# Performance work log

Measured on AMD Instinct MI355X. Metric: run time of the kernel, lower is better.

## Reference

```python
import jax, jax.numpy as jnp
import numpy as np

V = 100000          # vocab size
D = 256             # hidden dim
B, N = 32, 128      # batch, max_len
K = 100             # noise_ratio
NORM_TERM = 11.512925  # log(V), norm_term='auto'
BACKOFF_PROB = 1e-10


def setup_inputs() -> dict:
    key = jax.random.key(0)
    ks = jax.random.split(key, 6)
    target = jax.random.randint(ks[0], (B, N), 0, V)
    noise_samples = jax.random.randint(ks[1], (B, N, K), 0, V)
    hidden = jax.random.normal(ks[2], (B, N, D), dtype=jnp.float32) * 0.1
    weight = jax.random.normal(ks[3], (V, D), dtype=jnp.float32) * 0.05
    bias = jax.random.normal(ks[4], (V,), dtype=jnp.float32) * 0.01
    u = jax.random.uniform(ks[5], (V,), dtype=jnp.float32) + BACKOFF_PROB
    noise_probs = u / jnp.sum(u)  # normalized noise distribution
    return {"target": target, "noise_samples": noise_samples, "hidden": hidden,
            "weight": weight, "bias": bias, "noise_probs": noise_probs}


def reference(target, noise_samples, hidden, weight, bias, noise_probs):
    # score_noise = log P_noise(noise_samples)   (B,N,K) -- irregular gather on (V,)
    score_noise = jnp.log(noise_probs)[noise_samples]
    # get_score (IndexLinear): gathered output-embedding dot products
    w_t = weight[target]                                   # (B,N,D)
    score_model = jnp.einsum('bnd,bnd->bn', hidden, w_t) + bias[target] - NORM_TERM
    w_n = weight[noise_samples]                            # (B,N,K,D) big gather
    score_noise_in_model = (jnp.einsum('bnd,bnkd->bnk', hidden, w_n)
                            + bias[noise_samples] - NORM_TERM)
    # NCE binary classification loss (score_target_in_noise passed as zeros)
    log_k = jnp.log(jnp.float32(K))
    logit_true = score_model - log_k                        # (B,N) label=1
    logit_noise = score_noise_in_model - score_noise - log_k  # (B,N,K) label=0
    # BCE-with-logits: -log sigmoid(x) = softplus(-x); -log(1-sigmoid(x)) = softplus(x)
    loss = jax.nn.softplus(-logit_true) + jnp.sum(jax.nn.softplus(logit_noise), axis=-1)
    # reduction='elementwise_mean'
    return jnp.mean(loss)
```

## Files before the change

kernel.cpp:

```cpp
#include <hip/hip_runtime.h>
#include <math.h>

#define V 100000
#define D 256
#define B 32
#define N 128
#define K 100
#define NPOS (B * N)
#define NPAIR (NPOS * (K + 1))
#define BIN_ROWS 32
#define NBIN (V / BIN_ROWS)
#define NSHARD 16
#define CAP_S 32
#define MAXTOT (NSHARD * CAP_S)
#define ROW_W32 136
#define HVEC (NPOS * D / 4)
#define NORM_TERM 11.512925f
#define LOG_K 4.605170186f

typedef float    f32x4 __attribute__((ext_vector_type(4)));
typedef unsigned u32x2 __attribute__((ext_vector_type(2)));
typedef unsigned u32x4 __attribute__((ext_vector_type(4)));
typedef __fp16   f16x2 __attribute__((ext_vector_type(2)));

__device__ __forceinline__ float softplus(float x) {
    return fmaxf(x, 0.f) + __logf(1.f + __expf(-fabsf(x)));
}

__device__ __forceinline__ unsigned pack_f16(float a, float b) {
#if __has_builtin(__builtin_amdgcn_cvt_pkrtz)
    f16x2 h = __builtin_amdgcn_cvt_pkrtz(a, b);
#else
    f16x2 h; h.x = (__fp16)a; h.y = (__fp16)b;
#endif
    union { f16x2 h; unsigned u; } c; c.h = h;
    return c.u;
}

#if __has_builtin(__builtin_amdgcn_fdot2)
#define DOT2(a, b, c) __builtin_amdgcn_fdot2((a), (b), (c), false)
#else
__device__ __forceinline__ float DOT2(f16x2 a, f16x2 b, float c) {
    return fmaf((float)a.x, (float)b.x, fmaf((float)a.y, (float)b.y, c));
}
#endif

union V4H { u32x4 u; f16x2 h[4]; };

template <int CTRL>
__device__ __forceinline__ float dpp_add(float x) {
    int y = __builtin_amdgcn_update_dpp(__float_as_int(x), __float_as_int(x),
                                        CTRL, 0xF, 0xF, false);
    return x + __int_as_float(y);
}
__device__ __forceinline__ float quarter_sum(float x) {
    x = dpp_add<0xB1>(x);
    x = dpp_add<0x4E>(x);
    x = dpp_add<0x141>(x);
    x = dpp_add<0x140>(x);
    return x;
}

__global__ __launch_bounds__(256) void scatter_hconv_kernel(
    const int* __restrict__ target, const int* __restrict__ noise,
    const float* __restrict__ hidden,
    int* __restrict__ cursor, unsigned* __restrict__ buf,
    unsigned* __restrict__ htab32)
{
    const int p = blockIdx.x * 256 + threadIdx.x;

    int row, pos; unsigned flag;
    if (p < NPOS * K) { pos = p / K; row = noise[p]; flag = 0u; }
    else              { pos = p - NPOS * K; row = target[pos]; flag = 1u; }
    const int cell = (row >> 5) * NSHARD + (blockIdx.x & (NSHARD - 1));
    const int slot = atomicAdd(&cursor[cell], 1);
    if (slot < CAP_S)
        buf[(size_t)cell * CAP_S + slot] =
            ((unsigned)(row & (BIN_ROWS - 1)) << 13) | ((unsigned)pos << 1) | flag;

    if (p < HVEC) {
        const f32x4 h4 = *((const f32x4*)hidden + p);
        u32x2 o;
        o.x = pack_f16(h4.x, h4.y);
        o.y = pack_f16(h4.z, h4.w);
        *(u32x2*)(htab32 + (size_t)p * 2) = o;
    }
}

__global__ __launch_bounds__(256, 8) void compute_kernel(
    const unsigned* __restrict__ htab32, const float* __restrict__ weight,
    const float* __restrict__ bias, const float* __restrict__ noise_probs,
    const int* __restrict__ cursor, const unsigned* __restrict__ buf,
    float* __restrict__ out)
{
    __shared__ unsigned slab32[BIN_ROWS * ROW_W32];
    __shared__ float    sbias[BIN_ROWS];
    __shared__ float    slogp[BIN_ROWS];
    __shared__ unsigned plist[MAXTOT];
    __shared__ int      scnt[NSHARD];
    __shared__ int      pref[NSHARD + 1];
    __shared__ float    wsum[4];

    const int bin = blockIdx.x;
    const int tid = threadIdx.x;

    if (tid < NSHARD)
        scnt[tid] = min(cursor[bin * NSHARD + tid], CAP_S);
    __syncthreads();
    if (tid == 0) {
        int s = 0;
        #pragma unroll
        for (int i = 0; i < NSHARD; ++i) { pref[i] = s; s += scnt[i]; }
        pref[NSHARD] = s;
    }
    __syncthreads();
    const int total = pref[NSHARD];
    if (total == 0) return;

    const int wave = tid >> 6;
    const int lane = tid & 63;
    const int q    = lane >> 4;
    const int ql   = lane & 15;
    const int row0 = bin * BIN_ROWS;

    for (int r = wave; r < BIN_ROWS; r += 4) {
        const f32x4 w4 = __builtin_nontemporal_load(
            (const f32x4*)(weight + (size_t)(row0 + r) * D + lane * 4));
        u32x2 o;
        o.x = pack_f16(w4.x, w4.y);
        o.y = pack_f16(w4.z, w4.w);
        *(u32x2*)(slab32 + r * ROW_W32 + lane * 2) = o;
    }
    if (tid < BIN_ROWS) {
        sbias[tid] = bias[row0 + tid];
        slogp[tid] = __logf(noise_probs[row0 + tid]);
    }
    for (int i = tid; i < total; i += 256) {
        int s = 0;
        #pragma unroll
        for (int j = 1; j < NSHARD; ++j) s += (i >= pref[j]);
        plist[i] = buf[((size_t)(bin * NSHARD + s)) * CAP_S + (i - pref[s])];
    }
    __syncthreads();

    float loss = 0.f;
    for (int base = wave * 4; base < total; base += 16) {
        const int p = base + q;
        const bool valid = (p < total);
        const unsigned rec = valid ? plist[p] : 0u;
        const int rloc = (int)((rec >> 13) & (BIN_ROWS - 1));
        const int pos  = (int)((rec >> 1) & (NPOS - 1));

        const u32x4* hp = (const u32x4*)(htab32 + (size_t)pos * 128) + ql;
        V4H H0, H1, W0, W1;
        H0.u = hp[0];
        H1.u = hp[16];
        const unsigned* wr = slab32 + rloc * ROW_W32;
        W0.u = *(const u32x4*)(wr + ql * 4);
        W1.u = *(const u32x4*)(wr + 64 + ql * 4);

        float a0 = 0.f, a1 = 0.f, a2 = 0.f, a3 = 0.f;
        a0 = DOT2(H0.h[0], W0.h[0], a0);
        a1 = DOT2(H0.h[1], W0.h[1], a1);
        a2 = DOT2(H0.h[2], W0.h[2], a2);
        a3 = DOT2(H0.h[3], W0.h[3], a3);
        a0 = DOT2(H1.h[0], W1.h[0], a0);
        a1 = DOT2(H1.h[1], W1.h[1], a1);
        a2 = DOT2(H1.h[2], W1.h[2], a2);
        a3 = DOT2(H1.h[3], W1.h[3], a3);

        const float r = quarter_sum((a0 + a1) + (a2 + a3));

        const float score = r + sbias[rloc] - NORM_TERM;
        const float x = (rec & 1u) ? (LOG_K - score)
                                   : (score - slogp[rloc] - LOG_K);
        if (valid && ql == 0) loss += softplus(x);
    }

    loss += __shfl_xor(loss, 16, 64);
    loss += __shfl_xor(loss, 32, 64);
    if (lane == 0) wsum[wave] = loss;
    __syncthreads();
    if (tid == 0)
        atomicAdd(out, (wsum[0] + wsum[1] + wsum[2] + wsum[3])
                       * (1.0f / (float)NPOS));
}

extern "C" void kernel_launch(void* const* d_in, const int* in_sizes, int n_in,
                              void* d_out, int out_size, void* d_ws, size_t ws_size,
                              hipStream_t stream) {
    const int*   target      = (const int*)d_in[0];
    const int*   noise       = (const int*)d_in[1];
    const float* hidden      = (const float*)d_in[2];
    const float* weight      = (const float*)d_in[3];
    const float* bias        = (const float*)d_in[4];
    const float* noise_probs = (const float*)d_in[5];
    float* out = (float*)d_out;

    const size_t cursor_bytes = (size_t)NBIN * NSHARD * 4;
    const size_t buf_bytes    = (size_t)NBIN * NSHARD * CAP_S * 4;
    int*      cursor = (int*)d_ws;
    unsigned* buf    = (unsigned*)((char*)d_ws + cursor_bytes);
    unsigned* htab32 = (unsigned*)((char*)d_ws + cursor_bytes + buf_bytes);

    (void)hipMemsetAsync(cursor, 0, cursor_bytes, stream);
    (void)hipMemsetAsync(out, 0, sizeof(float), stream);

    scatter_hconv_kernel<<<NPAIR / 256, 256, 0, stream>>>(
        target, noise, hidden, cursor, buf, htab32);
    compute_kernel<<<NBIN, 256, 0, stream>>>(
        htab32, weight, bias, noise_probs, cursor, buf, out);
}
```

Before: 220.7 us.

## Process three bins per block with register-prefetched next weight slab

Each compute block now handles three consecutive bins instead of one. While it computes the current bin, it prefetches the next bin's weight rows and pair records into registers, then writes them to shared memory after a barrier. This is meant to hide global-load latency and cut per-block setup and launch overhead. In exchange it adds register pressure (occupancy bound lowered from 8 to 6 blocks), two barriers per bin and fewer blocks in the grid, and blocks can no longer exit early when a bin is empty.

```diff
diff --git a/kernel.cpp b/kernel.cpp
--- a/kernel.cpp
+++ b/kernel.cpp
@@ -13,6 +13,8 @@
 #define NSHARD 16
 #define CAP_S 32
 #define MAXTOT (NSHARD * CAP_S)
+#define BPB 3
+#define NBLK ((NBIN + BPB - 1) / BPB)
 #define ROW_W32 136
 #define HVEC (NPOS * D / 4)
 #define NORM_TERM 11.512925f
@@ -87,94 +89,143 @@
     }
 }
 
-__global__ __launch_bounds__(256, 8) void compute_kernel(
+__global__ __launch_bounds__(256, 6) void compute_kernel(
     const unsigned* __restrict__ htab32, const float* __restrict__ weight,
     const float* __restrict__ bias, const float* __restrict__ noise_probs,
     const int* __restrict__ cursor, const unsigned* __restrict__ buf,
     float* __restrict__ out)
 {
     __shared__ unsigned slab32[BIN_ROWS * ROW_W32];
-    __shared__ float    sbias[BIN_ROWS];
-    __shared__ float    slogp[BIN_ROWS];
+    __shared__ float    sbias[BPB * BIN_ROWS];
+    __shared__ float    slogp[BPB * BIN_ROWS];
     __shared__ unsigned plist[MAXTOT];
-    __shared__ int      scnt[NSHARD];
-    __shared__ int      pref[NSHARD + 1];
+    __shared__ int      scnt[BPB * NSHARD];
+    __shared__ int      pref[BPB][NSHARD + 1];
     __shared__ float    wsum[4];
 
-    const int bin = blockIdx.x;
+    const int b0  = blockIdx.x * BPB;
     const int tid = threadIdx.x;
-
-    if (tid < NSHARD)
-        scnt[tid] = min(cursor[bin * NSHARD + tid], CAP_S);
-    __syncthreads();
-    if (tid == 0) {
-        int s = 0;
-        #pragma unroll
-        for (int i = 0; i < NSHARD; ++i) { pref[i] = s; s += scnt[i]; }
-        pref[NSHARD] = s;
-    }
-    __syncthreads();
-    const int total = pref[NSHARD];
-    if (total == 0) return;
-
     const int wave = tid >> 6;
     const int lane = tid & 63;
     const int q    = lane >> 4;
     const int ql   = lane & 15;
-    const int row0 = bin * BIN_ROWS;
+
+    if (tid < BPB * NSHARD) {
+        const int j = tid >> 4, s = tid & 15, bin = b0 + j;
+        scnt[tid] = (bin < NBIN) ? min(cursor[bin * NSHARD + s], CAP_S) : 0;
+    }
+    __syncthreads();
+    if (tid < BPB) {
+        int s = 0;
+        #pragma unroll
+        for (int i = 0; i < NSHARD; ++i) { pref[tid][i] = s; s += scnt[tid * NSHARD + i]; }
+        pref[tid][NSHARD] = s;
+    }
+    __syncthreads();
 
     for (int r = wave; r < BIN_ROWS; r += 4) {
         const f32x4 w4 = __builtin_nontemporal_load(
-            (const f32x4*)(weight + (size_t)(row0 + r) * D + lane * 4));
+            (const f32x4*)(weight + (size_t)(b0 * BIN_ROWS + r) * D + lane * 4));
         u32x2 o;
         o.x = pack_f16(w4.x, w4.y);
         o.y = pack_f16(w4.z, w4.w);
         *(u32x2*)(slab32 + r * ROW_W32 + lane * 2) = o;
     }
-    if (tid < BIN_ROWS) {
-        sbias[tid] = bias[row0 + tid];
-        slogp[tid] = __logf(noise_probs[row0 + tid]);
-    }
-    for (int i = tid; i < total; i += 256) {
-        int s = 0;
-        #pragma unroll
-        for (int j = 1; j < NSHARD; ++j) s += (i >= pref[j]);
-        plist[i] = buf[((size_t)(bin * NSHARD + s)) * CAP_S + (i - pref[s])];
+    if (tid < BPB * BIN_ROWS) {
+        const int j = tid >> 5, r = tid & 31, bin = b0 + j;
+        if (bin < NBIN) {
+            sbias[tid] = bias[bin * BIN_ROWS + r];
+            slogp[tid] = __logf(noise_probs[bin * BIN_ROWS + r]);
+        }
+    }
+    {
+        const int total0 = pref[0][NSHARD];
+        for (int i = tid; i < total0; i += 256) {
+            int s = 0;
+            #pragma unroll
+            for (int m = 1; m < NSHARD; ++m) s += (i >= pref[0][m]);
+            plist[i] = buf[((size_t)(b0 * NSHARD + s)) * CAP_S + (i - pref[0][s])];
+        }
     }
     __syncthreads();
 
     float loss = 0.f;
-    for (int base = wave * 4; base < total; base += 16) {
-        const int p = base + q;
-        const bool valid = (p < total);
-        const unsigned rec = valid ? plist[p] : 0u;
-        const int rloc = (int)((rec >> 13) & (BIN_ROWS - 1));
-        const int pos  = (int)((rec >> 1) & (NPOS - 1));
-
-        const u32x4* hp = (const u32x4*)(htab32 + (size_t)pos * 128) + ql;
-        V4H H0, H1, W0, W1;
-        H0.u = hp[0];
-        H1.u = hp[16];
-        const unsigned* wr = slab32 + rloc * ROW_W32;
-        W0.u = *(const u32x4*)(wr + ql * 4);
-        W1.u = *(const u32x4*)(wr + 64 + ql * 4);
-
-        float a0 = 0.f, a1 = 0.f, a2 = 0.f, a3 = 0.f;
-        a0 = DOT2(H0.h[0], W0.h[0], a0);
-        a1 = DOT2(H0.h[1], W0.h[1], a1);
-        a2 = DOT2(H0.h[2], W0.h[2], a2);
-        a3 = DOT2(H0.h[3], W0.h[3], a3);
-        a0 = DOT2(H1.h[0], W1.h[0], a0);
-        a1 = DOT2(H1.h[1], W1.h[1], a1);
-        a2 = DOT2(H1.h[2], W1.h[2], a2);
-        a3 = DOT2(H1.h[3], W1.h[3], a3);
-
-        const float r = quarter_sum((a0 + a1) + (a2 + a3));
-
-        const float score = r + sbias[rloc] - NORM_TERM;
-        const float x = (rec & 1u) ? (LOG_K - score)
-                                   : (score - slogp[rloc] - LOG_K);
-        if (valid && ql == 0) loss += softplus(x);
+    for (int j = 0; j < BPB; ++j) {
+        const int bin   = b0 + j;
+        const int total = (bin < NBIN) ? pref[j][NSHARD] : 0;
+        const bool hasnext = (j + 1 < BPB) && (bin + 1 < NBIN);
+
+        f32x4 wpre[8];
+        if (hasnext) {
+            const float* wsrc = weight + (size_t)(bin + 1) * BIN_ROWS * D;
+            #pragma unroll
+            for (int i = 0; i < 8; ++i)
+                wpre[i] = __builtin_nontemporal_load(
+                    (const f32x4*)(wsrc + (size_t)(wave + 4 * i) * D + lane * 4));
+        }
+        unsigned pl_a = 0u, pl_b = 0u; int tot_n = 0;
+        if (hasnext) {
+            tot_n = pref[j + 1][NSHARD];
+            if (tid < tot_n) {
+                int s = 0;
+                #pragma unroll
+                for (int m = 1; m < NSHARD; ++m) s += (tid >= pref[j + 1][m]);
+                pl_a = buf[((size_t)((bin + 1) * NSHARD + s)) * CAP_S + (tid - pref[j + 1][s])];
+            }
+            if (tid + 256 < tot_n) {
+                int s = 0;
+                #pragma unroll
+                for (int m = 1; m < NSHARD; ++m) s += (tid + 256 >= pref[j + 1][m]);
+                pl_b = buf[((size_t)((bin + 1) * NSHARD + s)) * CAP_S + (tid + 256 - pref[j + 1][s])];
+            }
+        }
+
+        for (int base = wave * 4; base < total; base += 16) {
+            const int p = base + q;
+            const bool valid = (p < total);
+            const unsigned rec = valid ? plist[p] : 0u;
+            const int rloc = (int)((rec >> 13) & (BIN_ROWS - 1));
+            const int pos  = (int)((rec >> 1) & (NPOS - 1));
+
+            const u32x4* hp = (const u32x4*)(htab32 + (size_t)pos * 128) + ql;
+            V4H H0, H1, W0, W1;
+            H0.u = hp[0];
+            H1.u = hp[16];
+            const unsigned* wr = slab32 + rloc * ROW_W32;
+            W0.u = *(const u32x4*)(wr + ql * 4);
+            W1.u = *(const u32x4*)(wr + 64 + ql * 4);
+
+            float a0 = 0.f, a1 = 0.f, a2 = 0.f, a3 = 0.f;
+            a0 = DOT2(H0.h[0], W0.h[0], a0);
+            a1 = DOT2(H0.h[1], W0.h[1], a1);
+            a2 = DOT2(H0.h[2], W0.h[2], a2);
+            a3 = DOT2(H0.h[3], W0.h[3], a3);
+            a0 = DOT2(H1.h[0], W1.h[0], a0);
+            a1 = DOT2(H1.h[1], W1.h[1], a1);
+            a2 = DOT2(H1.h[2], W1.h[2], a2);
+            a3 = DOT2(H1.h[3], W1.h[3], a3);
+
+            const float r = quarter_sum((a0 + a1) + (a2 + a3));
+
+            const float score = r + sbias[j * BIN_ROWS + rloc] - NORM_TERM;
+            const float x = (rec & 1u) ? (LOG_K - score)
+                                       : (score - slogp[j * BIN_ROWS + rloc] - LOG_K);
+            if (valid && ql == 0) loss += softplus(x);
+        }
+        __syncthreads();
+
+        if (hasnext) {
+            #pragma unroll
+            for (int i = 0; i < 8; ++i) {
+                u32x2 o;
+                o.x = pack_f16(wpre[i].x, wpre[i].y);
+                o.y = pack_f16(wpre[i].z, wpre[i].w);
+                *(u32x2*)(slab32 + (wave + 4 * i) * ROW_W32 + lane * 2) = o;
+            }
+            if (tid < tot_n)       plist[tid]       = pl_a;
+            if (tid + 256 < tot_n) plist[tid + 256] = pl_b;
+        }
+        __syncthreads();
     }
 
     loss += __shfl_xor(loss, 16, 64);
@@ -208,6 +259,6 @@
 
     scatter_hconv_kernel<<<NPAIR / 256, 256, 0, stream>>>(
         target, noise, hidden, cursor, buf, htab32);
-    compute_kernel<<<NBIN, 256, 0, stream>>>(
+    compute_kernel<<<NBLK, 256, 0, stream>>>(
         htab32, weight, bias, noise_probs, cursor, buf, out);
 }
```

Measured after the change: 207.6 us. 6.0% less time.
